# Kernel tuning notes

Hardware: AMD Instinct MI355X
Metric: run time of the kernel (lower is better)

The kernel has to match this reference:

```python
import jax, jax.numpy as jnp
import numpy as np

D_MODEL = 1024
NUM_HEADS = 16
D_K = D_MODEL // NUM_HEADS


def setup_inputs() -> dict:
    key = jax.random.key(0)
    ks = jax.random.split(key, 10)
    s = 1.0 / np.sqrt(D_MODEL)  # ~ torch Linear init scale
    inp = {
        "x": jax.random.normal(ks[0], (2, 2048, D_MODEL), dtype=jnp.float32),
        "Wq": jax.random.uniform(ks[1], (D_MODEL, D_MODEL), jnp.float32, -s, s),
        "bq": jax.random.uniform(ks[2], (D_MODEL,), jnp.float32, -s, s),
        "Wk": jax.random.uniform(ks[3], (D_MODEL, D_MODEL), jnp.float32, -s, s),
        "bk": jax.random.uniform(ks[4], (D_MODEL,), jnp.float32, -s, s),
        "Wv": jax.random.uniform(ks[5], (D_MODEL, D_MODEL), jnp.float32, -s, s),
        "bv": jax.random.uniform(ks[6], (D_MODEL,), jnp.float32, -s, s),
        "Wo": jax.random.uniform(ks[7], (D_MODEL, D_MODEL), jnp.float32, -s, s),
        "bo": jax.random.uniform(ks[8], (D_MODEL,), jnp.float32, -s, s),
        "ln_gamma": jnp.ones((D_MODEL,), jnp.float32),
        "ln_beta": jnp.zeros((D_MODEL,), jnp.float32),
    }
    return inp


def reference(x, Wq, bq, Wk, bk, Wv, bv, Wo, bo, ln_gamma, ln_beta):
    B, S, D = x.shape
    residual = x
    # LayerNorm (eps=1e-5 as torch default)
    mu = jnp.mean(x, axis=-1, keepdims=True)
    var = jnp.mean(jnp.square(x - mu), axis=-1, keepdims=True)
    xn = (x - mu) * jax.lax.rsqrt(var + 1e-5) * ln_gamma + ln_beta
    # QKV projections (torch Linear: y = x @ W^T + b) -> (B, H, S, d_k)
    def proj(W, b):
        return (xn @ W.T + b).reshape(B, S, NUM_HEADS, D_K).transpose(0, 2, 1, 3)
    Q, K, V = proj(Wq, bq), proj(Wk, bk), proj(Wv, bv)
    scores = jnp.einsum("bhqd,bhkd->bhqk", Q, K) / np.sqrt(D_K).astype(np.float32)
    attn = jax.nn.softmax(scores, axis=-1)  # (B, H, S, S); dropout is no-op (eval)
    context = jnp.einsum("bhqk,bhkd->bhqd", attn, V)
    context = context.transpose(0, 2, 1, 3).reshape(B, S, D)
    out = context @ Wo.T + bo
    return out + residual, attn.mean(axis=1)
```

## Files before the change

### kernel.cpp

```cpp
#include <hip/hip_runtime.h>
#include <stdint.h>
#include <stddef.h>

#define DEV static __device__ __forceinline__

typedef float f32x4 __attribute__((ext_vector_type(4)));
typedef float f32x16 __attribute__((ext_vector_type(16)));
typedef unsigned u32x4 __attribute__((ext_vector_type(4)));
typedef __bf16 bf16x8 __attribute__((ext_vector_type(8)));

DEV short f2bf(float f) {
  union { float f; unsigned u; } a; a.f = f;
  unsigned r = a.u + 0x7fffu + ((a.u >> 16) & 1u);
  return (short)(r >> 16);
}

DEV void gld_lds16(const void* g, void* lds) {
  __builtin_amdgcn_global_load_lds(
      (__attribute__((address_space(1))) void*)(void*)g,
      (__attribute__((address_space(3))) void*)lds, 16, 0, 0);
}

DEV f32x4 MFMA(bf16x8 a, bf16x8 b, f32x4 c) {
  return __builtin_amdgcn_mfma_f32_16x16x32_bf16(a, b, c, 0, 0, 0);
}
DEV f32x16 MFMA32(bf16x8 a, bf16x8 b, f32x16 c) {
  return __builtin_amdgcn_mfma_f32_32x32x16_bf16(a, b, c, 0, 0, 0);
}

DEV float ex2(float x) { return __builtin_amdgcn_exp2f(x); }

DEV unsigned cvtpk(float lo, float hi) {
  unsigned r;
  asm("v_cvt_pk_bf16_f32 %0, %1, %2" : "=v"(r) : "v"(lo), "v"(hi));
  return r;
}

DEV float xhalf_sum(float v) {
  float a = v, b = v;
  asm volatile("v_permlane32_swap_b32 %0, %1" : "+v"(a), "+v"(b));
  return a + b;
}

#define LOG2E 1.4426950408889634f


__global__ __launch_bounds__(256) void k_cvtw_ln(
    const float* __restrict__ w0, const float* __restrict__ w1,
    const float* __restrict__ w2, const float* __restrict__ w3,
    short* __restrict__ dst, const float* __restrict__ x,
    const float* __restrict__ g, const float* __restrict__ be,
    short* __restrict__ xn) {
  __shared__ float ps[4], pss[4];
  if (blockIdx.x < 4096) {
    int i = blockIdx.x * 256 + threadIdx.x;
    int sel = i >> 18;
    const float* src = sel == 0 ? w0 : sel == 1 ? w1 : sel == 2 ? w2 : w3;
    int off = (i & 0x3ffff) * 4;
    float4 v = *(const float4*)(src + off);
    short4 o4; o4.x = f2bf(v.x); o4.y = f2bf(v.y); o4.z = f2bf(v.z); o4.w = f2bf(v.w);
    *(short4*)(dst + (size_t)i * 4) = o4;
  } else {
    int row = blockIdx.x - 4096;
    int t = threadIdx.x;
    const float4* xr = (const float4*)(x + (size_t)row * 1024);
    float4 v = xr[t];
    float s = v.x + v.y + v.z + v.w;
    float ss = v.x * v.x + v.y * v.y + v.z * v.z + v.w * v.w;
#pragma unroll
    for (int o = 32; o; o >>= 1) { s += __shfl_down(s, o); ss += __shfl_down(ss, o); }
    int w = t >> 6, lane = t & 63;
    if (lane == 0) { ps[w] = s; pss[w] = ss; }
    __syncthreads();
    float st = ps[0] + ps[1] + ps[2] + ps[3];
    float sst = pss[0] + pss[1] + pss[2] + pss[3];
    float mean = st * (1.0f / 1024.0f);
    float var = sst * (1.0f / 1024.0f) - mean * mean;
    float rstd = rsqrtf(var + 1e-5f);
    float4 gv = ((const float4*)g)[t];
    float4 bv = ((const float4*)be)[t];
    short4 o4;
    o4.x = f2bf((v.x - mean) * rstd * gv.x + bv.x);
    o4.y = f2bf((v.y - mean) * rstd * gv.y + bv.y);
    o4.z = f2bf((v.z - mean) * rstd * gv.z + bv.z);
    o4.w = f2bf((v.w - mean) * rstd * gv.w + bv.w);
    ((short4*)(xn + (size_t)row * 1024))[t] = o4;
  }
}

__global__ __launch_bounds__(512, 1) void k_gemm_qkv(
    const short* __restrict__ xn, const short* __restrict__ wbf,
    const float* __restrict__ bq, const float* __restrict__ bk,
    const float* __restrict__ bv, short* __restrict__ q_ws,
    short* __restrict__ k_ws, short* __restrict__ vt_ws) {
  __shared__ __align__(16) short lds[3][16384];
  int t = threadIdx.x, lane = t & 63, w = t >> 6;
  int wr = w >> 2, wc = w & 3;
  int z = blockIdx.z;
  int row0 = blockIdx.y * 256, col0 = blockIdx.x * 256;
  const short* A = xn + (size_t)row0 * 1024;
  const short* Bw = wbf + (size_t)z * (1024 * 1024) + (size_t)col0 * 1024;

  const short *ap0, *ap1, *bp0, *bp1;
  {
    int c = t, r = c >> 2, j = (c & 3) ^ (r & 3);
    ap0 = A + (size_t)r * 1024 + j * 8;
    bp0 = Bw + (size_t)r * 1024 + j * 8;
  }
  {
    int c = t + 512, r = c >> 2, j = (c & 3) ^ (r & 3);
    ap1 = A + (size_t)r * 1024 + j * 8;
    bp1 = Bw + (size_t)r * 1024 + j * 8;
  }

#define STGG(s_)                                                     \
  {                                                                  \
    short* at_ = lds[(s_) % 3];                                      \
    short* bt_ = lds[(s_) % 3] + 8192;                               \
    gld_lds16(ap0 + (s_) * 32, &at_[t * 8]);                         \
    gld_lds16(ap1 + (s_) * 32, &at_[(t + 512) * 8]);                 \
    gld_lds16(bp0 + (s_) * 32, &bt_[t * 8]);                         \
    gld_lds16(bp1 + (s_) * 32, &bt_[(t + 512) * 8]);                 \
  }

  int aoff[8], boff[4];
#pragma unroll
  for (int mi = 0; mi < 8; mi++) {
    int row = wr * 128 + mi * 16 + (lane & 15);
    aoff[mi] = row * 32 + (((lane >> 4) ^ (row & 3)) * 8);
  }
#pragma unroll
  for (int ni = 0; ni < 4; ni++) {
    int row = wc * 64 + ni * 16 + (lane & 15);
    boff[ni] = row * 32 + (((lane >> 4) ^ (row & 3)) * 8);
  }

  f32x4 acc[8][4];
#pragma unroll
  for (int m = 0; m < 8; m++)
#pragma unroll
    for (int n = 0; n < 4; n++) acc[m][n] = (f32x4)0.0f;

  STGG(0);
  for (int s = 0; s < 32; ++s) {
    STGG(s + 1 <= 31 ? s + 1 : 31);
    asm volatile("s_waitcnt vmcnt(4)" ::: "memory");
    __builtin_amdgcn_s_barrier();

    const short* at = lds[s % 3];
    const short* bt = lds[s % 3] + 8192;
    bf16x8 af[8], bf[4];
#pragma unroll
    for (int m = 0; m < 8; m++) af[m] = *(const bf16x8*)&at[aoff[m]];
#pragma unroll
    for (int n = 0; n < 4; n++) bf[n] = *(const bf16x8*)&bt[boff[n]];
    __builtin_amdgcn_s_setprio(1);
#pragma unroll
    for (int m = 0; m < 8; m++)
#pragma unroll
      for (int n = 0; n < 4; n++) acc[m][n] = MFMA(af[m], bf[n], acc[m][n]);
    __builtin_amdgcn_s_setprio(0);
  }

  if (z < 2) {
    const float* bias = z == 0 ? bq : bk;
    short* dst = z == 0 ? q_ws : k_ws;
    float scal = z == 0 ? (0.125f * LOG2E) : 1.0f;
#pragma unroll
    for (int m = 0; m < 8; m++)
#pragma unroll
      for (int n = 0; n < 4; n++)
#pragma unroll
        for (int r = 0; r < 4; r++) {
          int grow = row0 + wr * 128 + m * 16 + (lane >> 4) * 4 + r;
          int gcol = col0 + wc * 64 + n * 16 + (lane & 15);
          float val = (acc[m][n][r] + bias[gcol]) * scal;
          int bb = grow >> 11, sr = grow & 2047, h = gcol >> 6, d = gcol & 63;
          dst[(((size_t)bb * 16 + h) * 2048 + sr) * 64 + d] = f2bf(val);
        }
  } else {
    asm volatile("s_waitcnt vmcnt(0)" ::: "memory");
    __syncthreads();
    short* tb = &lds[0][0];
    int bb = row0 >> 11, s0 = row0 & 2047;
#pragma unroll
    for (int p = 0; p < 2; p++) {
      if (wr == p) {
#pragma unroll
        for (int m = 0; m < 8; m++)
#pragma unroll
          for (int n = 0; n < 4; n++)
#pragma unroll
            for (int r = 0; r < 4; r++) {
              int sl = m * 16 + (lane >> 4) * 4 + r;
              int d = n * 16 + (lane & 15);
              int gcol = col0 + wc * 64 + d;
              tb[wc * 8704 + d * 136 + sl] = f2bf(acc[m][n][r] + bv[gcol]);
            }
      }
      __syncthreads();
#pragma unroll
      for (int i = 0; i < 8; i++) {
        int c = t + i * 512;
        int hh = c >> 10, d = (c >> 4) & 63, sc = (c & 15) * 8;
        bf16x8 vv = *(const bf16x8*)&tb[hh * 8704 + d * 136 + sc];
        int bh = bb * 16 + (col0 >> 6) + hh;
        *(bf16x8*)&vt_ws[((size_t)bh * 64 + d) * 2048 + s0 + p * 128 + sc] = vv;
      }
      __syncthreads();
    }
  }
}

__global__ __launch_bounds__(256, 2) void k_attn1(
    const short* __restrict__ q_ws, const short* __restrict__ k_ws,
    const short* __restrict__ vt_ws, short* __restrict__ o_ws,
    float* __restrict__ l_ws) {
  __shared__ __align__(16) short k_lds[4][64 * 64];
  __shared__ __align__(16) short vt_lds[5][64 * 64];
  int t = threadIdx.x, lane = t & 63, w = t >> 6;
  int hi = lane >> 5, l31 = lane & 31;
  int flat = blockIdx.x + 16 * blockIdx.y + 256 * blockIdx.z;
  int mm = (flat & 7) * 64 + (flat >> 3);
  int qt = mm & 15, hd = (mm >> 4) & 15, b = mm >> 8;
  int bh = b * 16 + hd;
  int q0 = qt * 128;
  const short* qb = q_ws + (size_t)bh * (2048 * 64);
  const short* kb = k_ws + (size_t)bh * (2048 * 64);
  const short* vtb = vt_ws + (size_t)bh * (64 * 2048);
  int qg = q0 + w * 32 + l31;

  bf16x8 qf[4];
#pragma unroll
  for (int d4 = 0; d4 < 4; d4++)
    qf[d4] = *(const bf16x8*)&qb[(size_t)qg * 64 + d4 * 16 + hi * 8];
  asm volatile("s_waitcnt vmcnt(0)" ::: "memory");

  const short *kp0, *kp1, *vp0, *vp1;
  {
    int c = t, r = c >> 3, j = (c & 7) ^ (r & 7);
    kp0 = kb + (size_t)r * 64 + j * 8;
    vp0 = vtb + (size_t)r * 2048 + j * 8;
  }
  {
    int c = t + 256, r = c >> 3, j = (c & 7) ^ (r & 7);
    kp1 = kb + (size_t)r * 64 + j * 8;
    vp1 = vtb + (size_t)r * 2048 + j * 8;
  }

  int koff[8];
#pragma unroll
  for (int d4 = 0; d4 < 4; d4++) {
    int row0 = l31, row1 = 32 + l31;
    koff[2 * d4]     = row0 * 64 + (((d4 * 2 + hi) ^ (row0 & 7)) * 8);
    koff[2 * d4 + 1] = row1 * 64 + (((d4 * 2 + hi) ^ (row1 & 7)) * 8);
  }

#define STG(tl_)                                                         \
  {                                                                      \
    gld_lds16(kp0 + (size_t)(tl_) * 4096, &k_lds[(tl_) & 3][t * 8]);     \
    gld_lds16(kp1 + (size_t)(tl_) * 4096, &k_lds[(tl_) & 3][(t + 256) * 8]); \
    gld_lds16(vp0 + (size_t)(tl_) * 64, &vt_lds[(tl_) % 5][t * 8]);      \
    gld_lds16(vp1 + (size_t)(tl_) * 64, &vt_lds[(tl_) % 5][(t + 256) * 8]); \
  }

  STG(0);
  STG(1);

  f32x16 Oacc[2];
#pragma unroll
  for (int i = 0; i < 16; i++) { Oacc[0][i] = 0.0f; Oacc[1][i] = 0.0f; }
  float lrun = 0.0f;
  bf16x8 pb[4];

  for (int it = 0; it < 32; ++it) {
    int tn = it + 2 <= 31 ? it + 2 : 31;
    STG(tn);
    asm volatile("s_waitcnt vmcnt(8)" ::: "memory");
    __builtin_amdgcn_s_barrier();

    const short* kl = k_lds[it & 3];
    const short* vl = vt_lds[(it + 4) % 5];

    bf16x8 kfr[8], vfr[8];
#pragma unroll
    for (int i = 0; i < 8; i++) kfr[i] = *(const bf16x8*)&kl[koff[i]];
#pragma unroll
    for (int i = 0; i < 8; i++) vfr[i] = *(const bf16x8*)&vl[koff[i]];

    __builtin_amdgcn_s_setprio(1);
    f32x16 S0 = (f32x16)0.0f, S1 = (f32x16)0.0f;
#pragma unroll
    for (int d4 = 0; d4 < 4; d4++) {
      S0 = MFMA32(kfr[2 * d4], qf[d4], S0);
      S1 = MFMA32(kfr[2 * d4 + 1], qf[d4], S1);
    }
    if (it) {
#pragma unroll
      for (int ks = 0; ks < 4; ks++) {
        Oacc[0] = MFMA32(vfr[2 * ks], pb[ks], Oacc[0]);
        Oacc[1] = MFMA32(vfr[2 * ks + 1], pb[ks], Oacc[1]);
      }
    }
    __builtin_amdgcn_s_setprio(0);

    float rs0 = 0.0f, rs1 = 0.0f;
#pragma unroll
    for (int i = 0; i < 16; i++) {
      float p0 = ex2(S0[i]);
      float p1 = ex2(S1[i]);
      S0[i] = p0; S1[i] = p1;
      rs0 += p0; rs1 += p1;
    }
    lrun += xhalf_sum(rs0 + rs1);

#pragma unroll
    for (int ks = 0; ks < 4; ks++) {
      unsigned wA, wB, wC, wD;
      if (ks == 0) {
        wA = cvtpk(S0[0], S0[1]);  wB = cvtpk(S0[2], S0[3]);
        wC = cvtpk(S0[4], S0[5]);  wD = cvtpk(S0[6], S0[7]);
      } else if (ks == 1) {
        wA = cvtpk(S0[8], S0[9]);  wB = cvtpk(S0[10], S0[11]);
        wC = cvtpk(S0[12], S0[13]); wD = cvtpk(S0[14], S0[15]);
      } else if (ks == 2) {
        wA = cvtpk(S1[0], S1[1]);  wB = cvtpk(S1[2], S1[3]);
        wC = cvtpk(S1[4], S1[5]);  wD = cvtpk(S1[6], S1[7]);
      } else {
        wA = cvtpk(S1[8], S1[9]);  wB = cvtpk(S1[10], S1[11]);
        wC = cvtpk(S1[12], S1[13]); wD = cvtpk(S1[14], S1[15]);
      }
      asm volatile("v_permlane32_swap_b32 %0, %1" : "+v"(wA), "+v"(wC));
      asm volatile("v_permlane32_swap_b32 %0, %1" : "+v"(wB), "+v"(wD));
      u32x4 uu; uu.x = wA; uu.y = wB; uu.z = wC; uu.w = wD;
      pb[ks] = __builtin_bit_cast(bf16x8, uu);
    }
  }
  asm volatile("s_waitcnt vmcnt(0)" ::: "memory");
  __builtin_amdgcn_s_barrier();

  {
    const short* vl = vt_lds[1];
    __builtin_amdgcn_s_setprio(1);
#pragma unroll
    for (int ks = 0; ks < 4; ks++) {
      Oacc[0] = MFMA32(*(const bf16x8*)&vl[koff[2 * ks]], pb[ks], Oacc[0]);
      Oacc[1] = MFMA32(*(const bf16x8*)&vl[koff[2 * ks + 1]], pb[ks], Oacc[1]);
    }
    __builtin_amdgcn_s_setprio(0);
  }

  float rl = 1.0f / lrun;
  if (lane < 32) {
    l_ws[bh * 2048 + qg] = rl;
  }
#pragma unroll
  for (int dt = 0; dt < 2; dt++)
#pragma unroll
    for (int g = 0; g < 4; g++) {
      short4 o4;
      o4.x = f2bf(Oacc[dt][g * 4 + 0] * rl);
      o4.y = f2bf(Oacc[dt][g * 4 + 1] * rl);
      o4.z = f2bf(Oacc[dt][g * 4 + 2] * rl);
      o4.w = f2bf(Oacc[dt][g * 4 + 3] * rl);
      int d = dt * 32 + g * 8 + hi * 4;
      *(short4*)&o_ws[((size_t)(b * 2048 + qg)) * 1024 + hd * 64 + d] = o4;
    }
}

__global__ __launch_bounds__(256) void k_tail(
    const short* __restrict__ q_ws, const short* __restrict__ k_ws,
    const float* __restrict__ l_ws, float* __restrict__ out1,
    const short* __restrict__ o_ws, const short* __restrict__ wo_bf,
    const float* __restrict__ bo, const float* __restrict__ x,
    float* __restrict__ out0) {
  __shared__ __align__(16) char smem[3 * 16384 + 3 * 256];
  int t = threadIdx.x, lane = t & 63, w = t >> 6;

  if (blockIdx.x < 256) {
    short* at = (short*)smem;
    short* bt = (short*)(smem + 8192);
    int wr = w >> 1, wc = w & 1;
    int fo = blockIdx.x;
    int col0 = (fo & 7) * 128, row0 = (fo >> 3) * 128;
    const short* A = o_ws + (size_t)row0 * 1024;
    const short* Bw = wo_bf + (size_t)col0 * 1024;
    f32x4 acc[4][4];
#pragma unroll
    for (int m = 0; m < 4; m++)
#pragma unroll
      for (int n = 0; n < 4; n++) acc[m][n] = (f32x4)0.0f;

    for (int k0 = 0; k0 < 1024; k0 += 32) {
#pragma unroll
      for (int i = 0; i < 2; i++) {
        int c = t + i * 256;
        int r = c >> 2, cc = (c & 3) * 8;
        gld_lds16(A + (size_t)r * 1024 + k0 + cc, &at[c * 8]);
        gld_lds16(Bw + (size_t)r * 1024 + k0 + cc, &bt[c * 8]);
      }
      __syncthreads();
      bf16x8 af[4], bfr[4];
#pragma unroll
      for (int m = 0; m < 4; m++)
        af[m] = *(const bf16x8*)&at[(wr * 64 + m * 16 + (lane & 15)) * 32 + (lane >> 4) * 8];
#pragma unroll
      for (int n = 0; n < 4; n++)
        bfr[n] = *(const bf16x8*)&bt[(wc * 64 + n * 16 + (lane & 15)) * 32 + (lane >> 4) * 8];
#pragma unroll
      for (int m = 0; m < 4; m++)
#pragma unroll
        for (int n = 0; n < 4; n++) acc[m][n] = MFMA(af[m], bfr[n], acc[m][n]);
      __syncthreads();
    }
#pragma unroll
    for (int m = 0; m < 4; m++)
#pragma unroll
      for (int n = 0; n < 4; n++)
#pragma unroll
        for (int r = 0; r < 4; r++) {
          int grow = row0 + wr * 64 + m * 16 + (lane >> 4) * 4 + r;
          int gcol = col0 + wc * 64 + n * 16 + (lane & 15);
          float val = acc[m][n][r] + bo[gcol] + x[(size_t)grow * 1024 + gcol];
          out0[(size_t)grow * 1024 + gcol] = val;
        }
  } else {
    short* k_lds2 = (short*)smem;
    float* l_lds = (float*)(smem + 49152);
    int flat = blockIdx.x - 256;
    int mm = (flat & 7) * 128 + (flat >> 3);
    int q0 = (mm & 31) * 64, k2 = ((mm >> 5) & 15) * 128, b = mm >> 9;

    f32x4 pacc[8];
#pragma unroll
    for (int n = 0; n < 8; n++) pacc[n] = (f32x4)0.0f;

    int qrow = q0 + w * 16 + (lane & 15);
    size_t qoff0 = (size_t)qrow * 64 + (lane >> 4) * 8;
    const short* qb0 = q_ws + (size_t)(b * 16) * (2048 * 64);

#define STAGE2(hh)                                                               \
    {                                                                            \
      int bh_ = b * 16 + (hh);                                                   \
      const short* kb_ = k_ws + (size_t)bh_ * (2048 * 64);                       \
      short* kdst_ = k_lds2 + ((hh) % 3) * (128 * 64);                           \
      _Pragma("unroll")                                                          \
      for (int i = 0; i < 4; i++) {                                              \
        int c = t + i * 256;                                                     \
        int r = c >> 3, j = (c & 7) ^ (r & 7);                                   \
        gld_lds16(kb_ + (size_t)(k2 + r) * 64 + j * 8, &kdst_[c * 8]);           \
      }                                                                          \
      int cc = w * 4 + (t & 63);                                                 \
      if ((t & 63) < 4) {                                                        \
        gld_lds16(&l_ws[(size_t)bh_ * 2048 + q0 + cc * 4],                       \
                  &l_lds[((hh) % 3) * 64 + cc * 4]);                             \
      }                                                                          \
    }

    STAGE2(0);
    for (int h = 0; h < 16; ++h) {
      bf16x8 qf0 = *(const bf16x8*)&qb0[(size_t)h * (2048 * 64) + qoff0];
      bf16x8 qf1 = *(const bf16x8*)&qb0[(size_t)h * (2048 * 64) + qoff0 + 32];
      int hn = h < 15 ? h + 1 : 15;
      STAGE2(hn);
      asm volatile("s_waitcnt vmcnt(5)" ::: "memory");
      __builtin_amdgcn_s_barrier();

      const short* kl = k_lds2 + (h % 3) * (128 * 64);
      f32x4 sc[8];
#pragma unroll
      for (int n = 0; n < 8; n++) sc[n] = (f32x4)0.0f;
#pragma unroll
      for (int kf = 0; kf < 2; kf++)
#pragma unroll
        for (int n = 0; n < 8; n++) {
          int row = n * 16 + (lane & 15);
          bf16x8 kfr = *(const bf16x8*)&kl[row * 64 + (((kf * 4 + (lane >> 4)) ^ (row & 7)) * 8)];
          sc[n] = MFMA(kf == 0 ? qf0 : qf1, kfr, sc[n]);
        }
      f32x4 lh = *(const f32x4*)&l_lds[(h % 3) * 64 + w * 16 + (lane >> 4) * 4];
#pragma unroll
      for (int n = 0; n < 8; n++)
#pragma unroll
        for (int r = 0; r < 4; r++)
          pacc[n][r] += ex2(sc[n][r]) * lh[r];
    }

#pragma unroll
    for (int n = 0; n < 8; n++)
#pragma unroll
      for (int r = 0; r < 4; r++) {
        int q = q0 + w * 16 + (lane >> 4) * 4 + r;
        int k = k2 + n * 16 + (lane & 15);
        out1[((size_t)b * 2048 + q) * 2048 + k] = pacc[n][r] * 0.0625f;
      }
  }
}

extern "C" void kernel_launch(void* const* d_in, const int* in_sizes, int n_in,
                              void* d_out, int out_size, void* d_ws, size_t ws_size,
                              hipStream_t stream) {
  (void)in_sizes; (void)n_in; (void)out_size; (void)ws_size;
  const float* x   = (const float*)d_in[0];
  const float* Wq  = (const float*)d_in[1];
  const float* bq  = (const float*)d_in[2];
  const float* Wk  = (const float*)d_in[3];
  const float* bk  = (const float*)d_in[4];
  const float* Wv  = (const float*)d_in[5];
  const float* bv  = (const float*)d_in[6];
  const float* Wo  = (const float*)d_in[7];
  const float* bo  = (const float*)d_in[8];
  const float* lng = (const float*)d_in[9];
  const float* lnb = (const float*)d_in[10];
  float* out0 = (float*)d_out;
  float* out1 = out0 + (size_t)2 * 2048 * 1024;

  char* ws = (char*)d_ws;
  short* xn    = (short*)(ws);
  short* q_ws  = (short*)(ws + 8388608);
  short* k_ws  = (short*)(ws + 16777216);
  short* o_ws  = (short*)(ws + 25165824);
  short* vt_ws = (short*)(ws + 33554432);
  short* wbf   = (short*)(ws + 41943040);
  float* l_ws  = (float*)(ws + 50331648);

  k_cvtw_ln<<<8192, 256, 0, stream>>>(Wq, Wk, Wv, Wo, wbf, x, lng, lnb, xn);
  k_gemm_qkv<<<dim3(4, 16, 3), 512, 0, stream>>>(xn, wbf, bq, bk, bv, q_ws, k_ws, vt_ws);
  k_attn1<<<dim3(16, 16, 2), 256, 0, stream>>>(q_ws, k_ws, vt_ws, o_ws, l_ws);
  k_tail<<<1280, 256, 0, stream>>>(q_ws, k_ws, l_ws, out1,
                                   o_ws, wbf + (size_t)3 * 1024 * 1024, bo, x, out0);
}
```

Baseline: 155.3 us.

## Double query rows per attention-mean block and prefetch next head's Q fragments

The attention-mean part of the tail kernel now handles 128 query rows per block instead of 64, with two 16-row M-tiles per wave. Each K tile staged in LDS is reused across twice as many queries, which halves the block count for that part and the total K reads from global memory. Q fragments for the next head are also loaded one iteration ahead so their latency overlaps with compute, and the waitcnt is adjusted to match. The cost is higher register use (pacc doubles), which the launch bounds change to one block per CU acknowledges; that may lower occupancy.

```diff
diff --git a/kernel.cpp b/kernel.cpp
--- a/kernel.cpp
+++ b/kernel.cpp
@@ -368,13 +368,13 @@
     }
 }
 
-__global__ __launch_bounds__(256) void k_tail(
+__global__ __launch_bounds__(256, 1) void k_tail(
     const short* __restrict__ q_ws, const short* __restrict__ k_ws,
     const float* __restrict__ l_ws, float* __restrict__ out1,
     const short* __restrict__ o_ws, const short* __restrict__ wo_bf,
     const float* __restrict__ bo, const float* __restrict__ x,
     float* __restrict__ out0) {
-  __shared__ __align__(16) char smem[3 * 16384 + 3 * 256];
+  __shared__ __align__(16) char smem[3 * 16384 + 3 * 512];
   int t = threadIdx.x, lane = t & 63, w = t >> 6;
 
   if (blockIdx.x < 256) {
@@ -428,15 +428,17 @@
     short* k_lds2 = (short*)smem;
     float* l_lds = (float*)(smem + 49152);
     int flat = blockIdx.x - 256;
-    int mm = (flat & 7) * 128 + (flat >> 3);
-    int q0 = (mm & 31) * 64, k2 = ((mm >> 5) & 15) * 128, b = mm >> 9;
-
-    f32x4 pacc[8];
-#pragma unroll
-    for (int n = 0; n < 8; n++) pacc[n] = (f32x4)0.0f;
-
-    int qrow = q0 + w * 16 + (lane & 15);
-    size_t qoff0 = (size_t)qrow * 64 + (lane >> 4) * 8;
+    int mm = (flat & 7) * 64 + (flat >> 3);
+    int q0 = (mm & 15) * 128, k2 = ((mm >> 4) & 15) * 128, b = mm >> 8;
+
+    f32x4 pacc[2][8];
+#pragma unroll
+    for (int m = 0; m < 2; m++)
+#pragma unroll
+      for (int n = 0; n < 8; n++) pacc[m][n] = (f32x4)0.0f;
+
+    int qrow0 = q0 + w * 32 + (lane & 15);
+    size_t qoff0 = (size_t)qrow0 * 64 + (lane >> 4) * 8;
     const short* qb0 = q_ws + (size_t)(b * 16) * (2048 * 64);
 
 #define STAGE2(hh)                                                               \
@@ -450,50 +452,67 @@
         int r = c >> 3, j = (c & 7) ^ (r & 7);                                   \
         gld_lds16(kb_ + (size_t)(k2 + r) * 64 + j * 8, &kdst_[c * 8]);           \
       }                                                                          \
-      int cc = w * 4 + (t & 63);                                                 \
-      if ((t & 63) < 4) {                                                        \
+      int cc = w * 8 + (t & 63);                                                 \
+      if ((t & 63) < 8) {                                                        \
         gld_lds16(&l_ws[(size_t)bh_ * 2048 + q0 + cc * 4],                       \
-                  &l_lds[((hh) % 3) * 64 + cc * 4]);                             \
+                  &l_lds[((hh) % 3) * 128 + cc * 4]);                            \
       }                                                                          \
     }
 
+    bf16x8 qc00 = *(const bf16x8*)&qb0[qoff0];
+    bf16x8 qc01 = *(const bf16x8*)&qb0[qoff0 + 32];
+    bf16x8 qc10 = *(const bf16x8*)&qb0[qoff0 + 16 * 64];
+    bf16x8 qc11 = *(const bf16x8*)&qb0[qoff0 + 16 * 64 + 32];
     STAGE2(0);
+    bf16x8 qn00, qn01, qn10, qn11;
     for (int h = 0; h < 16; ++h) {
-      bf16x8 qf0 = *(const bf16x8*)&qb0[(size_t)h * (2048 * 64) + qoff0];
-      bf16x8 qf1 = *(const bf16x8*)&qb0[(size_t)h * (2048 * 64) + qoff0 + 32];
       int hn = h < 15 ? h + 1 : 15;
       STAGE2(hn);
-      asm volatile("s_waitcnt vmcnt(5)" ::: "memory");
+      {
+        size_t qb_h = (size_t)hn * (2048 * 64);
+        qn00 = *(const bf16x8*)&qb0[qb_h + qoff0];
+        qn01 = *(const bf16x8*)&qb0[qb_h + qoff0 + 32];
+        qn10 = *(const bf16x8*)&qb0[qb_h + qoff0 + 16 * 64];
+        qn11 = *(const bf16x8*)&qb0[qb_h + qoff0 + 16 * 64 + 32];
+      }
+      asm volatile("s_waitcnt vmcnt(12)" ::: "memory");
       __builtin_amdgcn_s_barrier();
 
       const short* kl = k_lds2 + (h % 3) * (128 * 64);
-      f32x4 sc[8];
-#pragma unroll
-      for (int n = 0; n < 8; n++) sc[n] = (f32x4)0.0f;
+      f32x4 sc0[8], sc1[8];
+#pragma unroll
+      for (int n = 0; n < 8; n++) { sc0[n] = (f32x4)0.0f; sc1[n] = (f32x4)0.0f; }
 #pragma unroll
       for (int kf = 0; kf < 2; kf++)
 #pragma unroll
         for (int n = 0; n < 8; n++) {
           int row = n * 16 + (lane & 15);
           bf16x8 kfr = *(const bf16x8*)&kl[row * 64 + (((kf * 4 + (lane >> 4)) ^ (row & 7)) * 8)];
-          sc[n] = MFMA(kf == 0 ? qf0 : qf1, kfr, sc[n]);
+          sc0[n] = MFMA(kf == 0 ? qc00 : qc01, kfr, sc0[n]);
+          sc1[n] = MFMA(kf == 0 ? qc10 : qc11, kfr, sc1[n]);
         }
-      f32x4 lh = *(const f32x4*)&l_lds[(h % 3) * 64 + w * 16 + (lane >> 4) * 4];
+      f32x4 lh0 = *(const f32x4*)&l_lds[(h % 3) * 128 + w * 32 + (lane >> 4) * 4];
+      f32x4 lh1 = *(const f32x4*)&l_lds[(h % 3) * 128 + w * 32 + 16 + (lane >> 4) * 4];
 #pragma unroll
       for (int n = 0; n < 8; n++)
 #pragma unroll
-        for (int r = 0; r < 4; r++)
-          pacc[n][r] += ex2(sc[n][r]) * lh[r];
-    }
-
-#pragma unroll
-    for (int n = 0; n < 8; n++)
-#pragma unroll
-      for (int r = 0; r < 4; r++) {
-        int q = q0 + w * 16 + (lane >> 4) * 4 + r;
-        int k = k2 + n * 16 + (lane & 15);
-        out1[((size_t)b * 2048 + q) * 2048 + k] = pacc[n][r] * 0.0625f;
-      }
+        for (int r = 0; r < 4; r++) {
+          pacc[0][n][r] += ex2(sc0[n][r]) * lh0[r];
+          pacc[1][n][r] += ex2(sc1[n][r]) * lh1[r];
+        }
+      qc00 = qn00; qc01 = qn01; qc10 = qn10; qc11 = qn11;
+    }
+
+#pragma unroll
+    for (int m = 0; m < 2; m++)
+#pragma unroll
+      for (int n = 0; n < 8; n++)
+#pragma unroll
+        for (int r = 0; r < 4; r++) {
+          int q = q0 + w * 32 + m * 16 + (lane >> 4) * 4 + r;
+          int k = k2 + n * 16 + (lane & 15);
+          out1[((size_t)b * 2048 + q) * 2048 + k] = pacc[m][n][r] * 0.0625f;
+        }
   }
 }
 
@@ -527,6 +546,6 @@
   k_cvtw_ln<<<8192, 256, 0, stream>>>(Wq, Wk, Wv, Wo, wbf, x, lng, lnb, xn);
   k_gemm_qkv<<<dim3(4, 16, 3), 512, 0, stream>>>(xn, wbf, bq, bk, bv, q_ws, k_ws, vt_ws);
   k_attn1<<<dim3(16, 16, 2), 256, 0, stream>>>(q_ws, k_ws, vt_ws, o_ws, l_ws);
-  k_tail<<<1280, 256, 0, stream>>>(q_ws, k_ws, l_ws, out1,
-                                   o_ws, wbf + (size_t)3 * 1024 * 1024, bo, x, out0);
-}
+  k_tail<<<768, 256, 0, stream>>>(q_ws, k_ws, l_ws, out1,
+                                  o_ws, wbf + (size_t)3 * 1024 * 1024, bo, x, out0);
+}
```

New measurement: 160.2 us. +3.2%, slower.
